# Kernel optimization log

Measured on AMD Instinct MI355X. Metric: run time of the kernel, lower is better.

The kernel has to match this reference:

```python
import jax, jax.numpy as jnp
import numpy as np

B, L, D = 4, 2048, 256
H, DH, MLP, MAX_REL = 8, 32, 1024, 16
LN_EPS = 1e-5


def _layernorm(x, g, b):
    mu = jnp.mean(x, axis=-1, keepdims=True)
    var = jnp.mean(jnp.square(x - mu), axis=-1, keepdims=True)
    return (x - mu) * jax.lax.rsqrt(var + LN_EPS) * g + b


def setup_inputs() -> dict:
    key = jax.random.key(0)
    ks = jax.random.split(key, 16)
    s = 0.02
    return {
        "x": jax.random.normal(ks[0], (B, L, D), jnp.float32),
        "key_padding_mask": jax.random.randint(ks[1], (B, L), 0, 2).astype(bool),
        "Wqkv": jax.random.normal(ks[2], (D, 3 * D), jnp.float32) * s,
        "bqkv": jnp.zeros((3 * D,), jnp.float32),
        "Wo": jax.random.normal(ks[3], (D, D), jnp.float32) * s,
        "bo": jnp.zeros((D,), jnp.float32),
        "ln1_g": jnp.ones((D,), jnp.float32),
        "ln1_b": jnp.zeros((D,), jnp.float32),
        "W1": jax.random.normal(ks[4], (D, MLP), jnp.float32) * s,
        "b1": jnp.zeros((MLP,), jnp.float32),
        "W2": jax.random.normal(ks[5], (MLP, D), jnp.float32) * s,
        "b2": jnp.zeros((D,), jnp.float32),
        "ln2_g": jnp.ones((D,), jnp.float32),
        "ln2_b": jnp.zeros((D,), jnp.float32),
        "rel_bias": jax.random.normal(ks[6], (2 * MAX_REL + 1, H), jnp.float32) * 0.01,
    }


def reference(x, key_padding_mask, Wqkv, bqkv, Wo, bo, ln1_g, ln1_b,
              W1, b1, W2, b2, ln2_g, ln2_b, rel_bias):
    Bx, Lw, Dm = x.shape
    scale = DH ** -0.5
    qkv = x @ Wqkv + bqkv                                   # [B,L,3D]
    q, k, v = jnp.split(qkv, 3, axis=-1)
    q = q.reshape(Bx, Lw, H, DH).transpose(0, 2, 1, 3)      # [B,H,L,dh]
    k = k.reshape(Bx, Lw, H, DH).transpose(0, 2, 1, 3)
    v = v.reshape(Bx, Lw, H, DH).transpose(0, 2, 1, 3)
    scores = jnp.einsum("bhqd,bhkd->bhqk", q, k) * scale    # [B,H,L,L]
    idx = jnp.arange(Lw)
    rel_clip = jnp.clip(idx[None, :] - idx[:, None], -MAX_REL, MAX_REL) + MAX_REL
    bias = rel_bias[rel_clip].transpose(2, 0, 1)            # [H,L,L]
    scores = scores + bias[None]
    scores = jnp.where(key_padding_mask[:, None, None, :], jnp.float32(-1e9), scores)
    attn = jax.nn.softmax(scores, axis=-1)                  # dropout = identity (eval)
    out = jnp.einsum("bhqk,bhkd->bhqd", attn, v)
    out = out.transpose(0, 2, 1, 3).reshape(Bx, Lw, Dm)
    out = out @ Wo + bo
    x = _layernorm(x + out, ln1_g, ln1_b)
    m = jax.nn.relu(x @ W1 + b1) @ W2 + b2
    x = _layernorm(x + m, ln2_g, ln2_b)
    return x
```

## Files before the change

### kernel.cpp

```cpp
#include <hip/hip_runtime.h>

#define B_   4
#define L_   2048
#define D_   256
#define H_   8
#define DH_  32
#define MLP_ 1024
#define LOG2E 1.4426950408889634f

typedef __attribute__((ext_vector_type(8))) short  short8;
typedef __attribute__((ext_vector_type(4))) float  f32x4;
typedef __attribute__((ext_vector_type(2))) float  f32x2;
typedef unsigned long long ull;

union FragU { short8 v; struct { ull lo, hi; } q; unsigned u[4]; };
union SU { f32x4 v4; f32x2 v2[2]; };

__device__ __forceinline__ unsigned short f2bf(float f) {
  unsigned u = __float_as_uint(f);
  u += 0x7fffu + ((u >> 16) & 1u);
  return (unsigned short)(u >> 16);
}

__device__ __forceinline__ ull pack4(float a, float b, float c, float d) {
  return (ull)f2bf(a) | ((ull)f2bf(b) << 16) | ((ull)f2bf(c) << 32) | ((ull)f2bf(d) << 48);
}

__device__ __forceinline__ unsigned cvt_pk_bf16(float lo, float hi) {
  unsigned r;
  asm("v_cvt_pk_bf16_f32 %0, %1, %2" : "=v"(r) : "v"(lo), "v"(hi));
  return r;
}

__device__ __forceinline__ f32x2 pk_add(f32x2 a, f32x2 b) {
  f32x2 r; asm("v_pk_add_f32 %0, %1, %2" : "=v"(r) : "v"(a), "v"(b)); return r;
}

__device__ __forceinline__ float fexp2(float x) {
#if __has_builtin(__builtin_amdgcn_exp2f)
  return __builtin_amdgcn_exp2f(x);
#else
  return exp2f(x);
#endif
}

#define GLL16(gp, lp) __builtin_amdgcn_global_load_lds( \
    (const __attribute__((address_space(1))) void*)(gp), \
    (__attribute__((address_space(3))) void*)(lp), 16, 0, 0)

__launch_bounds__(256)
__global__ void prep_all(const float* __restrict__ x,
                         const int* __restrict__ mask, const float* __restrict__ relb,
                         const float* __restrict__ Wqkv, const float* __restrict__ Wo,
                         const float* __restrict__ W1, const float* __restrict__ W2,
                         unsigned short* __restrict__ xb,
                         float* __restrict__ maskf,
                         float* __restrict__ mlo, float* __restrict__ mhi,
                         unsigned short* __restrict__ wqkvt, unsigned short* __restrict__ wot,
                         unsigned short* __restrict__ w1t, unsigned short* __restrict__ w2t) {
  __shared__ float tile[32][33];
  const int bid = blockIdx.x;
  if (bid < 768) {
    const float* src; unsigned short* dst; int R, C, tr, tc;
    if (bid < 192)      { src = Wqkv; dst = wqkvt; R = 256;  C = 768;  tr = bid / 24;          tc = bid % 24; }
    else if (bid < 256) { src = Wo;   dst = wot;   R = 256;  C = 256;  tr = (bid - 192) >> 3;  tc = (bid - 192) & 7; }
    else if (bid < 512) { src = W1;   dst = w1t;   R = 256;  C = 1024; tr = (bid - 256) >> 5;  tc = (bid - 256) & 31; }
    else                { src = W2;   dst = w2t;   R = 1024; C = 256;  tr = (bid - 512) >> 3;  tc = (bid - 512) & 7; }
    const int tx = threadIdx.x & 31, ty = threadIdx.x >> 5;
#pragma unroll
    for (int i = 0; i < 4; ++i) {
      const int r = tr * 32 + ty + i * 8;
      tile[ty + i * 8][tx] = src[(size_t)r * C + tc * 32 + tx];
    }
    __syncthreads();
#pragma unroll
    for (int i = 0; i < 4; ++i) {
      const int c = tc * 32 + ty + i * 8;
      dst[(size_t)c * R + tr * 32 + tx] = f2bf(tile[tx][ty + i * 8]);
    }
  } else {
    const int i = (bid - 768) * 256 + threadIdx.x;
    if (i < 524288) {
      const float4 v = *(const float4*)(x + (size_t)i * 4);
      *(ull*)(xb + (size_t)i * 4) = pack4(v.x, v.y, v.z, v.w);
    } else if (i < 532480) {
      const int j = i - 524288;
      maskf[j] = mask[j] ? -1e9f : 0.f;
    } else {
      const int j2 = i - 532480;
      const int t = j2 >> 16, idx = j2 & 65535;
      const int bh = idx >> 11, j = idx & 2047;
      const int bq = bh >> 3, h = bh & 7;
      const float base = mask[bq * L_ + j] ? -1e9f : 0.f;
      const float bias = relb[(t ? 32 * H_ : 0) + h] * LOG2E;
      (t ? mhi : mlo)[idx] = base + bias;
    }
  }
}

template <int MODE, int TM, int TN, int NBX, int BYG>
__launch_bounds__(256)
__global__ void gemm_k(const unsigned short* __restrict__ A,
                       const unsigned short* __restrict__ Bt,
                       const float* __restrict__ bias,
                       unsigned short* __restrict__ outb0,
                       unsigned short* __restrict__ outb1,
                       unsigned short* __restrict__ outb2,
                       int K)
{
  constexpr int MI = TM / 32, NI = TN / 32;
  __shared__ alignas(16) unsigned short As[2][TM * 64];
  __shared__ alignas(16) unsigned short Bs[2][TN * 64];
  const int tid  = threadIdx.x;
  const int lane = tid & 63, wv = tid >> 6;
  const int wr = wv >> 1, wc = wv & 1;
  const int lr = lane & 15, g = lane >> 4;
  const int bid = blockIdx.x;
  const int xcd = bid & 7, ii = bid >> 3;
  const int by = xcd * BYG + ii / NBX;
  const int bx = ii % NBX;
  const int m0 = by * TM, n0 = bx * TN;
  const int l8 = lane >> 3, jj = lane & 7;

  auto stage = [&](int buf, int k0) {
#pragma unroll
    for (int i = 0; i < MI; ++i) {
      const int row = i * 32 + wv * 8 + l8;
      GLL16(A + (size_t)(m0 + row) * K + k0 + ((jj ^ (row & 7)) * 8),
            &As[buf][i * 2048 + wv * 512]);
    }
#pragma unroll
    for (int i = 0; i < NI; ++i) {
      const int row = i * 32 + wv * 8 + l8;
      GLL16(Bt + (size_t)(n0 + row) * K + k0 + ((jj ^ (row & 7)) * 8),
            &Bs[buf][i * 2048 + wv * 512]);
    }
  };

  f32x4 acc[MI][NI];
#pragma unroll
  for (int i = 0; i < MI; ++i)
#pragma unroll
    for (int j = 0; j < NI; ++j) acc[i][j] = (f32x4)(0.f);

  stage(0, 0);
  for (int k0 = 0; k0 < K; k0 += 64) {
    const int cur = (k0 >> 6) & 1;
    if (k0 + 64 < K) {
      stage(cur ^ 1, k0 + 64);
      asm volatile("s_waitcnt vmcnt(%0)" :: "n"(MI + NI) : "memory");
    } else {
      asm volatile("s_waitcnt vmcnt(0)" ::: "memory");
    }
    __builtin_amdgcn_sched_barrier(0);
    __builtin_amdgcn_s_barrier();
#pragma unroll
    for (int kk = 0; kk < 2; ++kk) {
      FragU af[MI], bf[NI];
#pragma unroll
      for (int mi = 0; mi < MI; ++mi) {
        const int row = wr * (TM / 2) + mi * 16 + lr;
        const int sw = (row & 7) << 3;
        af[mi].v = *(const short8*)&As[cur][row * 64 + ((kk * 32 + 8 * g) ^ sw)];
      }
#pragma unroll
      for (int ni = 0; ni < NI; ++ni) {
        const int row = wc * (TN / 2) + ni * 16 + lr;
        const int sw = (row & 7) << 3;
        bf[ni].v = *(const short8*)&Bs[cur][row * 64 + ((kk * 32 + 8 * g) ^ sw)];
      }
#pragma unroll
      for (int mi = 0; mi < MI; ++mi)
#pragma unroll
        for (int ni = 0; ni < NI; ++ni)
          acc[mi][ni] = __builtin_amdgcn_mfma_f32_16x16x32_bf16(af[mi].v, bf[ni].v, acc[mi][ni], 0, 0, 0);
    }
    asm volatile("s_waitcnt lgkmcnt(0)" ::: "memory");
    __builtin_amdgcn_sched_barrier(0);
    __builtin_amdgcn_s_barrier();
  }

#pragma unroll
  for (int mi = 0; mi < MI; ++mi) {
#pragma unroll
    for (int ni = 0; ni < NI; ++ni) {
      const int n = n0 + wc * (TN / 2) + ni * 16 + lr;
      const float bv = bias[n];
#pragma unroll
      for (int r = 0; r < 4; ++r) {
        const int m = m0 + wr * (TM / 2) + mi * 16 + 4 * g + r;
        float val = acc[mi][ni][r] + bv;
        if constexpr (MODE == 0) {
          const int s = n >> 8, hh = (n >> 5) & 7, dh = n & 31;
          const int bb = m >> 11, l = m & (L_ - 1);
          if (s == 0) {
            outb0[((size_t)(bb * H_ + hh) * L_ + l) * DH_ + dh] =
                f2bf(val * (0.17677669529663687f * LOG2E));
          } else if (s == 1) {
            outb1[((size_t)(bb * H_ + hh) * L_ + l) * DH_ + dh] = f2bf(val);
          } else {
            outb2[((size_t)(bb * H_ + hh) * DH_ + dh) * L_ + l] = f2bf(val);
          }
        } else {
          outb0[(size_t)m * MLP_ + n] = f2bf(fmaxf(val, 0.f));
        }
      }
    }
  }
}

template <bool WRITE_BF>
__launch_bounds__(512)
__global__ void gemmln_k(const unsigned short* __restrict__ A,
                         const unsigned short* __restrict__ Bt,
                         const float* __restrict__ bias,
                         const float* __restrict__ resid,
                         const float* __restrict__ lng,
                         const float* __restrict__ lnb,
                         float* __restrict__ outf,
                         unsigned short* __restrict__ outb,
                         int K)
{
  __shared__ alignas(16) unsigned short As[2][16 * 64];
  __shared__ alignas(16) unsigned short Bs[2][256 * 64];
  __shared__ float rsum[8][16], rsq[8][16], rmu[16], rrstd[16];
  const int tid  = threadIdx.x;
  const int lane = tid & 63, wv = tid >> 6;
  const int lr = lane & 15, g = lane >> 4;
  const int m0 = blockIdx.x * 16;
  const int l8 = lane >> 3, jj = lane & 7;

  auto stage = [&](int buf, int k0) {
    if (wv < 2) {
      const int row = wv * 8 + l8;
      GLL16(A + (size_t)(m0 + row) * K + k0 + ((jj ^ (row & 7)) * 8),
            &As[buf][wv * 512]);
    }
#pragma unroll
    for (int i = 0; i < 4; ++i) {
      const int n = i * 64 + wv * 8 + l8;
      GLL16(Bt + (size_t)n * K + k0 + ((jj ^ (n & 7)) * 8),
            &Bs[buf][i * 4096 + wv * 512]);
    }
  };

  f32x4 acc[2];
  acc[0] = (f32x4)(0.f); acc[1] = (f32x4)(0.f);

  stage(0, 0);
  for (int k0 = 0; k0 < K; k0 += 64) {
    const int cur = (k0 >> 6) & 1;
    if (k0 + 64 < K) {
      stage(cur ^ 1, k0 + 64);
      asm volatile("s_waitcnt vmcnt(4)" ::: "memory");
    } else {
      asm volatile("s_waitcnt vmcnt(0)" ::: "memory");
    }
    __builtin_amdgcn_sched_barrier(0);
    __builtin_amdgcn_s_barrier();
#pragma unroll
    for (int kk = 0; kk < 2; ++kk) {
      FragU af, bf[2];
      {
        const int sw = (lr & 7) << 3;
        af.v = *(const short8*)&As[cur][lr * 64 + ((kk * 32 + 8 * g) ^ sw)];
      }
#pragma unroll
      for (int ni = 0; ni < 2; ++ni) {
        const int row = wv * 32 + ni * 16 + lr;
        const int sw = (row & 7) << 3;
        bf[ni].v = *(const short8*)&Bs[cur][row * 64 + ((kk * 32 + 8 * g) ^ sw)];
      }
#pragma unroll
      for (int ni = 0; ni < 2; ++ni)
        acc[ni] = __builtin_amdgcn_mfma_f32_16x16x32_bf16(af.v, bf[ni].v, acc[ni], 0, 0, 0);
    }
    asm volatile("s_waitcnt lgkmcnt(0)" ::: "memory");
    __builtin_amdgcn_sched_barrier(0);
    __builtin_amdgcn_s_barrier();
  }

  float g2[2], b2[2], bias2[2];
  int col[2];
#pragma unroll
  for (int ni = 0; ni < 2; ++ni) {
    col[ni] = wv * 32 + ni * 16 + lr;
    g2[ni] = lng[col[ni]]; b2[ni] = lnb[col[ni]]; bias2[ni] = bias[col[ni]];
  }
  float vals[2][4];
#pragma unroll
  for (int r = 0; r < 4; ++r) {
    const int row = 4 * g + r;
    float s = 0.f, q = 0.f;
#pragma unroll
    for (int ni = 0; ni < 2; ++ni) {
      float v = acc[ni][r] + bias2[ni] + resid[(size_t)(m0 + row) * D_ + col[ni]];
      vals[ni][r] = v; s += v; q += v * v;
    }
#pragma unroll
    for (int off = 1; off < 16; off <<= 1) {
      s += __shfl_xor(s, off); q += __shfl_xor(q, off);
    }
    if (lr == 0) { rsum[wv][row] = s; rsq[wv][row] = q; }
  }
  __syncthreads();
  if (tid < 16) {
    float s = 0.f, q = 0.f;
#pragma unroll
    for (int w = 0; w < 8; ++w) { s += rsum[w][tid]; q += rsq[w][tid]; }
    const float mu = s * (1.f / D_);
    rmu[tid] = mu;
    rrstd[tid] = rsqrtf(q * (1.f / D_) - mu * mu + 1e-5f);
  }
  __syncthreads();
#pragma unroll
  for (int r = 0; r < 4; ++r) {
    const int row = 4 * g + r;
    const float mu = rmu[row], rs = rrstd[row];
#pragma unroll
    for (int ni = 0; ni < 2; ++ni) {
      const float o = (vals[ni][r] - mu) * rs * g2[ni] + b2[ni];
      const size_t idx = (size_t)(m0 + row) * D_ + col[ni];
      outf[idx] = o;
      if constexpr (WRITE_BF) outb[idx] = f2bf(o);
    }
  }
}

__launch_bounds__(512)
__global__ void attn_k(const unsigned short* __restrict__ qb,
                       const unsigned short* __restrict__ kp,
                       const unsigned short* __restrict__ vT,
                       const float* __restrict__ maskf,
                       const float* __restrict__ mlo,
                       const float* __restrict__ mhi,
                       const float* __restrict__ relb,
                       unsigned short* __restrict__ aout)
{
  __shared__ alignas(16) unsigned short Ks[2][128 * 40];
  __shared__ alignas(16) unsigned short Vs[2][32 * 128];
  __shared__ alignas(16) float biasv[36];
  const int tid = threadIdx.x;
  const int lane = tid & 63, wv = tid >> 6;
  const int lr = lane & 15, g = lane >> 4;
  const int bid = blockIdx.x;
  const int ii = bid >> 3;
  const int bh = (bid & 7) * 4 + (ii >> 4);
  const int qblk = ii & 15;
  const int b = bh >> 3, h = bh & 7;
  const size_t bhoff = (size_t)bh * (L_ * DH_);
  if (tid < 33) biasv[tid] = relb[tid * H_ + h] * LOG2E;
  const int qw0 = qblk * 128 + wv * 16;

  FragU qf;
  qf.v = *(const short8*)(qb + bhoff + (size_t)(qw0 + lr) * DH_ + 8 * g);

  f32x4 O0 = (f32x4)(0.f), O1 = (f32x4)(0.f);
  f32x2 ssum2 = {0.f, 0.f};
  const f32x4 z4 = (f32x4)(0.f);
  const int krow = tid >> 2, koff = (tid & 3) * 8;
  const float* mtl = mlo + (size_t)bh * L_ + 4 * g;
  const float* mth = mhi + (size_t)bh * L_ + 4 * g;
  const float* mbn = maskf + (size_t)b * L_ + 4 * g;

  {
    const int4 ka = *(const int4*)(kp + bhoff + (size_t)krow * DH_ + koff);
    const int d = wv * 4 + (lane >> 4);
    GLL16(vT + ((size_t)bh * DH_ + d) * L_ + (((lane & 15) * 8) ^ ((d & 7) * 8)),
          &Vs[0][wv * 512]);
    *(int4*)&Ks[0][krow * 40 + koff] = ka;
    asm volatile("s_waitcnt vmcnt(0) lgkmcnt(0)" ::: "memory");
    __builtin_amdgcn_s_barrier();
  }

#pragma unroll 2
  for (int ch = 0; ch < 16; ++ch) {
    const int cur = ch & 1, nxt = cur ^ 1;
    const int kv = ch * 128;
    const bool more = ch < 15;
    int4 ka = {0, 0, 0, 0};
    if (more) {
      ka = *(const int4*)(kp + bhoff + (size_t)(kv + 128 + krow) * DH_ + koff);
      const int d = wv * 4 + (lane >> 4);
      GLL16(vT + ((size_t)bh * DH_ + d) * L_ + kv + 128 + (((lane & 15) * 8) ^ ((d & 7) * 8)),
            &Vs[nxt][wv * 512]);
    }

    SU sT[2][4];
#pragma unroll
    for (int st = 0; st < 2; ++st) {
      const unsigned short* KsC = &Ks[cur][st * 64 * 40];
#pragma unroll
      for (int jt = 0; jt < 4; ++jt) {
        FragU kf;
        kf.v = *(const short8*)&KsC[(jt * 16 + lr) * 40 + 8 * g];
        sT[st][jt].v4 = __builtin_amdgcn_mfma_f32_16x16x32_bf16(kf.v, qf.v, z4, 0, 0, 0);
      }
    }

#pragma unroll
    for (int st = 0; st < 2; ++st) {
      const int j0 = kv + st * 64;
      const int dlt = j0 - qw0;
      if (dlt >= 32 || dlt <= -80) {
        const float* mt = (dlt > 0) ? mth : mtl;
#pragma unroll
        for (int jt = 0; jt < 4; ++jt) {
          SU mk; mk.v4 = *(const f32x4*)(mt + j0 + jt * 16);
          sT[st][jt].v2[0] = pk_add(sT[st][jt].v2[0], mk.v2[0]);
          sT[st][jt].v2[1] = pk_add(sT[st][jt].v2[1], mk.v2[1]);
        }
      } else {
#pragma unroll
        for (int jt = 0; jt < 4; ++jt)
#pragma unroll
          for (int r = 0; r < 4; ++r) {
            int rel = j0 + jt * 16 + 4 * g + r - (qw0 + lr);
            rel = rel < -16 ? -16 : (rel > 16 ? 16 : rel);
            sT[st][jt].v4[r] += biasv[rel + 16] + mbn[j0 + jt * 16 + r];
          }
      }
#pragma unroll
      for (int jt = 0; jt < 4; ++jt)
#pragma unroll
        for (int r = 0; r < 4; ++r)
          sT[st][jt].v4[r] = fexp2(sT[st][jt].v4[r]);
      const f32x2 s01 = pk_add(sT[st][0].v2[0], sT[st][0].v2[1]);
      const f32x2 s23 = pk_add(sT[st][1].v2[0], sT[st][1].v2[1]);
      const f32x2 s45 = pk_add(sT[st][2].v2[0], sT[st][2].v2[1]);
      const f32x2 s67 = pk_add(sT[st][3].v2[0], sT[st][3].v2[1]);
      ssum2 = pk_add(ssum2, pk_add(pk_add(s01, s23), pk_add(s45, s67)));

      FragU a0, a1;
      a0.u[0] = cvt_pk_bf16(sT[st][0].v4[0], sT[st][0].v4[1]);
      a0.u[1] = cvt_pk_bf16(sT[st][0].v4[2], sT[st][0].v4[3]);
      a0.u[2] = cvt_pk_bf16(sT[st][1].v4[0], sT[st][1].v4[1]);
      a0.u[3] = cvt_pk_bf16(sT[st][1].v4[2], sT[st][1].v4[3]);
      a1.u[0] = cvt_pk_bf16(sT[st][2].v4[0], sT[st][2].v4[1]);
      a1.u[1] = cvt_pk_bf16(sT[st][2].v4[2], sT[st][2].v4[3]);
      a1.u[2] = cvt_pk_bf16(sT[st][3].v4[0], sT[st][3].v4[1]);
      a1.u[3] = cvt_pk_bf16(sT[st][3].v4[2], sT[st][3].v4[3]);

      FragU vf00, vf01, vf10, vf11;
#pragma unroll
      for (int dt = 0; dt < 2; ++dt) {
        const int row = dt * 16 + lr;
        const int sw = (row & 7) << 3;
        FragU v0, v1;
        v0.q.lo = *(const ull*)&Vs[cur][row * 128 + ((st * 64 + 4 * g) ^ sw)];
        v0.q.hi = *(const ull*)&Vs[cur][row * 128 + ((st * 64 + 16 + 4 * g) ^ sw)];
        v1.q.lo = *(const ull*)&Vs[cur][row * 128 + ((st * 64 + 32 + 4 * g) ^ sw)];
        v1.q.hi = *(const ull*)&Vs[cur][row * 128 + ((st * 64 + 48 + 4 * g) ^ sw)];
        if (dt == 0) { vf00 = v0; vf01 = v1; } else { vf10 = v0; vf11 = v1; }
      }
      O0 = __builtin_amdgcn_mfma_f32_16x16x32_bf16(a0.v, vf00.v, O0, 0, 0, 0);
      O0 = __builtin_amdgcn_mfma_f32_16x16x32_bf16(a1.v, vf01.v, O0, 0, 0, 0);
      O1 = __builtin_amdgcn_mfma_f32_16x16x32_bf16(a0.v, vf10.v, O1, 0, 0, 0);
      O1 = __builtin_amdgcn_mfma_f32_16x16x32_bf16(a1.v, vf11.v, O1, 0, 0, 0);
    }

    if (more) {
      *(int4*)&Ks[nxt][krow * 40 + koff] = ka;
    }
    asm volatile("s_waitcnt vmcnt(0) lgkmcnt(0)" ::: "memory");
    __builtin_amdgcn_sched_barrier(0);
    __builtin_amdgcn_s_barrier();
  }

  float ssum = ssum2[0] + ssum2[1];
  ssum += __shfl_xor(ssum, 16);
  ssum += __shfl_xor(ssum, 32);
#pragma unroll
  for (int r = 0; r < 4; ++r) {
    const float sden = __shfl(ssum, 4 * g + r);
    const float inv = 1.f / sden;
    const int qo = qw0 + 4 * g + r;
    unsigned short* orow = aout + ((size_t)(b * L_ + qo)) * D_ + h * DH_;
    orow[lr]      = f2bf(O0[r] * inv);
    orow[16 + lr] = f2bf(O1[r] * inv);
  }
}

extern "C" void kernel_launch(void* const* d_in, const int* in_sizes, int n_in,
                              void* d_out, int out_size, void* d_ws, size_t ws_size,
                              hipStream_t stream) {
  (void)in_sizes; (void)n_in; (void)out_size; (void)ws_size;
  const float* x    = (const float*)d_in[0];
  const int*   mask = (const int*)d_in[1];
  const float* Wqkv = (const float*)d_in[2];
  const float* bqkv = (const float*)d_in[3];
  const float* Wo   = (const float*)d_in[4];
  const float* bo   = (const float*)d_in[5];
  const float* ln1g = (const float*)d_in[6];
  const float* ln1b = (const float*)d_in[7];
  const float* W1   = (const float*)d_in[8];
  const float* b1   = (const float*)d_in[9];
  const float* W2   = (const float*)d_in[10];
  const float* b2   = (const float*)d_in[11];
  const float* ln2g = (const float*)d_in[12];
  const float* ln2b = (const float*)d_in[13];
  const float* relb = (const float*)d_in[14];

  size_t off = 0;
  char* wsb = (char*)d_ws;
  auto carve = [&](size_t bytes) -> void* {
    void* p = wsb + off;
    off += (bytes + 255) & ~(size_t)255;
    return p;
  };
  const size_t tokb = (size_t)B_ * L_;
  unsigned short* xb    = (unsigned short*)carve(tokb * D_ * 2);
  unsigned short* qbuf  = (unsigned short*)carve(tokb * D_ * 2);
  unsigned short* kbuf  = (unsigned short*)carve(tokb * D_ * 2);
  unsigned short* vTb   = (unsigned short*)carve(tokb * D_ * 2);
  unsigned short* attnb = (unsigned short*)carve(tokb * D_ * 2);
  unsigned short* wqkvt = (unsigned short*)carve((size_t)3 * D_ * D_ * 2);
  unsigned short* wot   = (unsigned short*)carve((size_t)D_ * D_ * 2);
  unsigned short* w1t   = (unsigned short*)carve((size_t)D_ * MLP_ * 2);
  unsigned short* w2t   = (unsigned short*)carve((size_t)D_ * MLP_ * 2);
  float*          x1    = (float*)carve(tokb * D_ * 4);
  unsigned short* x1b   = (unsigned short*)carve(tokb * D_ * 2);
  unsigned short* hbuf  = (unsigned short*)carve(tokb * MLP_ * 2);
  float*          maskfb = (float*)carve(tokb * 4);
  float*          mlob  = (float*)carve((size_t)B_ * H_ * L_ * 4);
  float*          mhib  = (float*)carve((size_t)B_ * H_ * L_ * 4);

  prep_all<<<3360, 256, 0, stream>>>(x, mask, relb, Wqkv, Wo, W1, W2,
                                     xb, maskfb, mlob, mhib,
                                     wqkvt, wot, w1t, w2t);

  gemm_k<0, 64, 128, 6, 16><<<768, 256, 0, stream>>>(
      xb, wqkvt, bqkv, qbuf, kbuf, vTb, D_);
  attn_k<<<512, 512, 0, stream>>>(
      qbuf, kbuf, vTb, maskfb, mlob, mhib, relb, attnb);
  gemmln_k<true><<<tokb / 16, 512, 0, stream>>>(
      attnb, wot, bo, x, ln1g, ln1b, x1, x1b, D_);
  gemm_k<2, 64, 128, 8, 16><<<1024, 256, 0, stream>>>(
      x1b, w1t, b1, hbuf, nullptr, nullptr, D_);
  gemmln_k<false><<<tokb / 16, 512, 0, stream>>>(
      hbuf, w2t, b2, x1, ln2g, ln2b, (float*)d_out, nullptr, MLP_);
}
```

Baseline: 98.78 us.

## Vectorize V-transpose stores in QKV epilogue and single-buffer GEMM+LN smem

In the QKV GEMM epilogue, the four consecutive rows held by each lane for the transposed V output are packed into one 8-byte store instead of four scalar bf16 stores. The Q/K and MLP paths keep scalar stores but their index math is simplified. The GEMM+LayerNorm kernel drops its double-buffered shared-memory staging for a single buffer, waiting for each tile to finish loading before computing. That halves LDS use, which may allow more resident blocks, but it gives up the overlap of global loads with MFMA work.

```diff
diff --git a/kernel.cpp b/kernel.cpp
--- a/kernel.cpp
+++ b/kernel.cpp
@@ -186,24 +186,31 @@
     for (int ni = 0; ni < NI; ++ni) {
       const int n = n0 + wc * (TN / 2) + ni * 16 + lr;
       const float bv = bias[n];
-#pragma unroll
-      for (int r = 0; r < 4; ++r) {
-        const int m = m0 + wr * (TM / 2) + mi * 16 + 4 * g + r;
-        float val = acc[mi][ni][r] + bv;
-        if constexpr (MODE == 0) {
-          const int s = n >> 8, hh = (n >> 5) & 7, dh = n & 31;
-          const int bb = m >> 11, l = m & (L_ - 1);
-          if (s == 0) {
-            outb0[((size_t)(bb * H_ + hh) * L_ + l) * DH_ + dh] =
-                f2bf(val * (0.17677669529663687f * LOG2E));
-          } else if (s == 1) {
-            outb1[((size_t)(bb * H_ + hh) * L_ + l) * DH_ + dh] = f2bf(val);
-          } else {
-            outb2[((size_t)(bb * H_ + hh) * DH_ + dh) * L_ + l] = f2bf(val);
+      const int mrow = m0 + wr * (TM / 2) + mi * 16 + 4 * g;
+      if constexpr (MODE == 0) {
+        const int s = n >> 8, hh = (n >> 5) & 7, dh = n & 31;
+        const int bb = m0 >> 11;
+        if (s == 2) {
+          const int l0 = mrow & (L_ - 1);
+          *(ull*)&outb2[((size_t)(bb * H_ + hh) * DH_ + dh) * L_ + l0] =
+              pack4(acc[mi][ni][0] + bv, acc[mi][ni][1] + bv,
+                    acc[mi][ni][2] + bv, acc[mi][ni][3] + bv);
+        } else {
+#pragma unroll
+          for (int r = 0; r < 4; ++r) {
+            const int l = (mrow + r) & (L_ - 1);
+            const float val = acc[mi][ni][r] + bv;
+            if (s == 0)
+              outb0[((size_t)(bb * H_ + hh) * L_ + l) * DH_ + dh] =
+                  f2bf(val * (0.17677669529663687f * LOG2E));
+            else
+              outb1[((size_t)(bb * H_ + hh) * L_ + l) * DH_ + dh] = f2bf(val);
           }
-        } else {
-          outb0[(size_t)m * MLP_ + n] = f2bf(fmaxf(val, 0.f));
         }
+      } else {
+#pragma unroll
+        for (int r = 0; r < 4; ++r)
+          outb0[(size_t)(mrow + r) * MLP_ + n] = f2bf(fmaxf(acc[mi][ni][r] + bv, 0.f));
       }
     }
   }
@@ -221,8 +228,8 @@
                          unsigned short* __restrict__ outb,
                          int K)
 {
-  __shared__ alignas(16) unsigned short As[2][16 * 64];
-  __shared__ alignas(16) unsigned short Bs[2][256 * 64];
+  __shared__ alignas(16) unsigned short As[16 * 64];
+  __shared__ alignas(16) unsigned short Bs[256 * 64];
   __shared__ float rsum[8][16], rsq[8][16], rmu[16], rrstd[16];
   const int tid  = threadIdx.x;
   const int lane = tid & 63, wv = tid >> 6;
@@ -230,32 +237,22 @@
   const int m0 = blockIdx.x * 16;
   const int l8 = lane >> 3, jj = lane & 7;
 
-  auto stage = [&](int buf, int k0) {
+  f32x4 acc[2];
+  acc[0] = (f32x4)(0.f); acc[1] = (f32x4)(0.f);
+
+  for (int k0 = 0; k0 < K; k0 += 64) {
     if (wv < 2) {
       const int row = wv * 8 + l8;
       GLL16(A + (size_t)(m0 + row) * K + k0 + ((jj ^ (row & 7)) * 8),
-            &As[buf][wv * 512]);
+            &As[wv * 512]);
     }
 #pragma unroll
     for (int i = 0; i < 4; ++i) {
       const int n = i * 64 + wv * 8 + l8;
       GLL16(Bt + (size_t)n * K + k0 + ((jj ^ (n & 7)) * 8),
-            &Bs[buf][i * 4096 + wv * 512]);
-    }
-  };
-
-  f32x4 acc[2];
-  acc[0] = (f32x4)(0.f); acc[1] = (f32x4)(0.f);
-
-  stage(0, 0);
-  for (int k0 = 0; k0 < K; k0 += 64) {
-    const int cur = (k0 >> 6) & 1;
-    if (k0 + 64 < K) {
-      stage(cur ^ 1, k0 + 64);
-      asm volatile("s_waitcnt vmcnt(4)" ::: "memory");
-    } else {
-      asm volatile("s_waitcnt vmcnt(0)" ::: "memory");
-    }
+            &Bs[i * 4096 + wv * 512]);
+    }
+    asm volatile("s_waitcnt vmcnt(0)" ::: "memory");
     __builtin_amdgcn_sched_barrier(0);
     __builtin_amdgcn_s_barrier();
 #pragma unroll
@@ -263,13 +260,13 @@
       FragU af, bf[2];
       {
         const int sw = (lr & 7) << 3;
-        af.v = *(const short8*)&As[cur][lr * 64 + ((kk * 32 + 8 * g) ^ sw)];
+        af.v = *(const short8*)&As[lr * 64 + ((kk * 32 + 8 * g) ^ sw)];
       }
 #pragma unroll
       for (int ni = 0; ni < 2; ++ni) {
         const int row = wv * 32 + ni * 16 + lr;
         const int sw = (row & 7) << 3;
-        bf[ni].v = *(const short8*)&Bs[cur][row * 64 + ((kk * 32 + 8 * g) ^ sw)];
+        bf[ni].v = *(const short8*)&Bs[row * 64 + ((kk * 32 + 8 * g) ^ sw)];
       }
 #pragma unroll
       for (int ni = 0; ni < 2; ++ni)
```

Result: faster. 95.95 us (-2.9%).
